# Kernel optimization log

Hardware: AMD Instinct MI355X
Metric: run time of the kernel (lower is better)

The kernel has to match this reference:

```python
import jax, jax.numpy as jnp
import numpy as np

B, S, D, H, DFF = 8, 1024, 1024, 16, 4096
DK = D // H
EPS = 1e-5


def setup_inputs() -> dict:
    key = jax.random.key(0)
    ks = jax.random.split(key, 12)
    sc = lambda n: 1.0 / np.sqrt(n)
    return {
        "x": jax.random.normal(ks[0], (B, S, D), jnp.float32),
        "src_mask": jnp.ones((B, 1, 1, S), jnp.int32),
        "wq": jax.random.normal(ks[1], (D, D), jnp.float32) * sc(D),
        "bq": jnp.zeros((D,), jnp.float32),
        "wk": jax.random.normal(ks[2], (D, D), jnp.float32) * sc(D),
        "bk": jnp.zeros((D,), jnp.float32),
        "wv": jax.random.normal(ks[3], (D, D), jnp.float32) * sc(D),
        "bv": jnp.zeros((D,), jnp.float32),
        "wo": jax.random.normal(ks[4], (D, D), jnp.float32) * sc(D),
        "bo": jnp.zeros((D,), jnp.float32),
        "w1": jax.random.normal(ks[5], (DFF, D), jnp.float32) * sc(D),
        "b1": jnp.zeros((DFF,), jnp.float32),
        "w2": jax.random.normal(ks[6], (D, DFF), jnp.float32) * sc(DFF),
        "b2": jnp.zeros((D,), jnp.float32),
        "g1": jnp.ones((1,), jnp.float32),
        "be1": jnp.zeros((1,), jnp.float32),
        "g2": jnp.ones((1,), jnp.float32),
        "be2": jnp.zeros((1,), jnp.float32),
    }


def _layernorm(x, gamma, beta):
    # Faithful to source: torch.var defaults to unbiased (ddof=1); scalar gamma/beta.
    mu = jnp.mean(x, axis=-1, keepdims=True)
    var = jnp.var(x, axis=-1, keepdims=True, ddof=1)
    return gamma * (x - mu) / jnp.sqrt(var + EPS) + beta


def _mha(x, wq, bq, wk, bk, wv, bv, wo, bo):
    q = (x @ wq.T + bq).reshape(B, S, H, DK).transpose(0, 2, 1, 3)
    k = (x @ wk.T + bk).reshape(B, S, H, DK).transpose(0, 2, 1, 3)
    v = (x @ wv.T + bv).reshape(B, S, H, DK).transpose(0, 2, 1, 3)
    scores = jnp.einsum("bhqd,bhkd->bhqk", q, k) / np.sqrt(DK)
    # NOTE: source uses non-inplace masked_fill whose result is discarded,
    # so the mask has no effect on the executed math; we replicate that.
    attn = jax.nn.softmax(scores, axis=-1)
    out = jnp.einsum("bhqk,bhkd->bhqd", attn, v)
    out = out.transpose(0, 2, 1, 3).reshape(B, S, D)
    return out @ wo.T + bo


def reference(x, src_mask, wq, bq, wk, bk, wv, bv, wo, bo,
              w1, b1, w2, b2, g1, be1, g2, be2):
    # residual 1: pre-norm self-attention (dropout=0 in eval)
    x = x + _mha(_layernorm(x, g1, be1), wq, bq, wk, bk, wv, bv, wo, bo)
    # residual 2: pre-norm FFN
    h = _layernorm(x, g2, be2)
    ff = jax.nn.relu(h @ w1.T + b1) @ w2.T + b2
    return x + ff
```

## Files before the change

### kernel.cpp

```cpp
#include <hip/hip_runtime.h>

typedef unsigned short u16;
typedef unsigned int u32;
typedef __attribute__((ext_vector_type(8))) __bf16 bf16x8;
typedef __attribute__((ext_vector_type(4))) float f32x4;

#define B_ 8
#define S_ 1024
#define D_ 1024
#define H_ 16
#define DK_ 64
#define DFF_ 4096
#define LDQKV 3072

__device__ __forceinline__ float bflo(u32 u) { return __uint_as_float(u << 16); }
__device__ __forceinline__ float bfhi(u32 u) { return __uint_as_float(u & 0xffff0000u); }
__device__ __forceinline__ u16 f2bf(float f) {
    u32 u = __float_as_uint(f);
    u += 0x7fffu + ((u >> 16) & 1u);
    return (u16)(u >> 16);
}

__device__ __forceinline__ void gl2lds16(const u16* g, u16* l) {
    __builtin_amdgcn_global_load_lds(
        (const __attribute__((address_space(1))) void*)g,
        (__attribute__((address_space(3))) void*)l, 16, 0, 0);
}

__global__ __launch_bounds__(256) void sniff_kernel(const u16* __restrict__ w,
                                                    int* __restrict__ flag) {
    float mx = 0.f;
    for (int i = threadIdx.x; i < 4096; i += 256) {
        float v = fabsf(bflo((u32)w[i]));
        if (!isnan(v)) mx = fmaxf(mx, v);
    }
#pragma unroll
    for (int m = 1; m < 64; m <<= 1) mx = fmaxf(mx, __shfl_xor(mx, m, 64));
    __shared__ float wmx[4];
    if ((threadIdx.x & 63) == 0) wmx[threadIdx.x >> 6] = mx;
    __syncthreads();
    if (threadIdx.x == 0) {
        float m2 = fmaxf(fmaxf(wmx[0], wmx[1]), fmaxf(wmx[2], wmx[3]));
        *flag = (m2 > 1e3f) ? 1 : 0;
    }
}

__global__ __launch_bounds__(256) void norm_kernel(const void* __restrict__ in,
                                                   u16* __restrict__ out, int n,
                                                   const int* __restrict__ flag) {
    const int i = blockIdx.x * 256 + threadIdx.x;
    if (i >= n) return;
    if (*flag)
        out[i] = f2bf(((const float*)in)[i]);
    else
        out[i] = ((const u16*)in)[i];
}

struct SmallTbl {
    const void* src[10];
    u16* dst[10];
    int n[10];
};
__global__ __launch_bounds__(256) void norm_small(SmallTbl tb,
                                                  const int* __restrict__ flag) {
    int i = blockIdx.x * 256 + threadIdx.x;
    const int f = *flag;
#pragma unroll
    for (int j = 0; j < 10; ++j) {
        if (i < tb.n[j]) {
            if (f)
                tb.dst[j][i] = f2bf(((const float*)tb.src[j])[i]);
            else
                tb.dst[j][i] = ((const u16*)tb.src[j])[i];
            return;
        }
        i -= tb.n[j];
    }
}

template <int INF>
__global__ __launch_bounds__(256) void ln_kernel(const void* __restrict__ in,
                                                 const u16* __restrict__ gs,
                                                 const u16* __restrict__ bs,
                                                 u16* __restrict__ out,
                                                 const int* __restrict__ flag) {
    const int row = blockIdx.x, t = threadIdx.x;
    const bool f32in = (INF == 1) || (INF == 2 && flag[0] != 0);
    float v0, v1, v2, v3;
    if (f32in) {
        const float* p = (const float*)in + (size_t)row * D_ + t * 4;
        float4 f = *(const float4*)p;
        v0 = f.x; v1 = f.y; v2 = f.z; v3 = f.w;
    } else {
        const u16* p = (const u16*)in + (size_t)row * D_ + t * 4;
        uint2 u = *(const uint2*)p;
        v0 = bflo(u.x); v1 = bfhi(u.x); v2 = bflo(u.y); v3 = bfhi(u.y);
    }
    float s = v0 + v1 + v2 + v3;
    float sq = v0 * v0 + v1 * v1 + v2 * v2 + v3 * v3;
#pragma unroll
    for (int m = 1; m < 64; m <<= 1) {
        s += __shfl_xor(s, m, 64);
        sq += __shfl_xor(sq, m, 64);
    }
    __shared__ float ss[4], sqs[4];
    const int w = t >> 6;
    if ((t & 63) == 0) { ss[w] = s; sqs[w] = sq; }
    __syncthreads();
    s = ss[0] + ss[1] + ss[2] + ss[3];
    sq = sqs[0] + sqs[1] + sqs[2] + sqs[3];
    const float mu = s * (1.f / 1024.f);
    float var = (sq - 1024.f * mu * mu) * (1.f / 1023.f);
    var = fmaxf(var, 0.f);
    const float rstd = rsqrtf(var + 1e-5f);
    const float gm = bflo((u32)gs[0]);
    const float bt = bflo((u32)bs[0]);
    const float y0 = gm * (v0 - mu) * rstd + bt;
    const float y1 = gm * (v1 - mu) * rstd + bt;
    const float y2 = gm * (v2 - mu) * rstd + bt;
    const float y3 = gm * (v3 - mu) * rstd + bt;
    uint2 uo;
    uo.x = (u32)f2bf(y0) | ((u32)f2bf(y1) << 16);
    uo.y = (u32)f2bf(y2) | ((u32)f2bf(y3) << 16);
    *(uint2*)(out + (size_t)row * D_ + t * 4) = uo;
}

template <int RELU, int RES, int OUTF>
__global__ __launch_bounds__(256, 4) void gemm_bt(const u16* __restrict__ A,
                                                  const u16* __restrict__ W,
                                                  const u16* __restrict__ bias,
                                                  const void* __restrict__ res,
                                                  void* __restrict__ out,
                                                  int M, int N, int K,
                                                  const int* __restrict__ oflag) {
    __shared__ __align__(16) u16 As[128 * 64];
    __shared__ __align__(16) u16 Bs[128 * 64];
    const int t = threadIdx.x;
    const int lane = t & 63, w = t >> 6;
    const int wm = w >> 1, wn = w & 1;

    const int nx = N >> 7;
    const int gsz = nx << 3;
    const int id = blockIdx.x;
    const int grp = id / gsz;
    const int rem = id - grp * gsz;
    const int m0 = ((grp << 3) + (rem & 7)) << 7;
    const int n0 = (rem >> 3) << 7;

    f32x4 acc[4][4];
#pragma unroll
    for (int mi = 0; mi < 4; ++mi)
#pragma unroll
        for (int ni = 0; ni < 4; ++ni) acc[mi][ni] = (f32x4){0.f, 0.f, 0.f, 0.f};

    const int r8 = lane >> 3, s8 = lane & 7;
    const int cg = s8 ^ r8;
    const u16* Ag = A + (size_t)(m0 + w * 8 + r8) * K + cg * 8;
    const u16* Bg = W + (size_t)(n0 + w * 8 + r8) * K + cg * 8;
    const size_t rI = (size_t)32 * K;
    u16* Asd = &As[(w * 8) * 64];
    u16* Bsd = &Bs[(w * 8) * 64];

    const int c = lane & 15, g = lane >> 4;
    const u16* As_r = &As[(wm * 64 + c) * 64];
    const u16* Bs_r = &Bs[(wn * 64 + c) * 64];
    const int sl0 = (g ^ (c & 7)) * 8;
    const int sl1 = ((4 + g) ^ (c & 7)) * 8;

    for (int kt = 0; kt < K; kt += 64) {
        __syncthreads();
        gl2lds16(Ag, Asd);
        gl2lds16(Ag + rI, Asd + 32 * 64);
        gl2lds16(Ag + 2 * rI, Asd + 64 * 64);
        gl2lds16(Ag + 3 * rI, Asd + 96 * 64);
        gl2lds16(Bg, Bsd);
        gl2lds16(Bg + rI, Bsd + 32 * 64);
        gl2lds16(Bg + 2 * rI, Bsd + 64 * 64);
        gl2lds16(Bg + 3 * rI, Bsd + 96 * 64);
        Ag += 64; Bg += 64;
        __syncthreads();
#pragma unroll
        for (int kc = 0; kc < 2; ++kc) {
            const int sl = kc ? sl1 : sl0;
            bf16x8 af[4], bfr[4];
#pragma unroll
            for (int i = 0; i < 4; ++i) {
                af[i] = *(const bf16x8*)(As_r + i * 16 * 64 + sl);
                bfr[i] = *(const bf16x8*)(Bs_r + i * 16 * 64 + sl);
            }
#pragma unroll
            for (int mi = 0; mi < 4; ++mi)
#pragma unroll
                for (int ni = 0; ni < 4; ++ni)
                    acc[mi][ni] = __builtin_amdgcn_mfma_f32_16x16x32_bf16(af[mi], bfr[ni], acc[mi][ni], 0, 0, 0);
        }
    }

    const int fl = oflag ? oflag[0] : 0;
    const bool f32o = (OUTF == 1) || (OUTF == 2 && fl != 0);
    const int qd = lane >> 4, cl = lane & 15;
#pragma unroll
    for (int ni = 0; ni < 4; ++ni) {
        const int col = n0 + wn * 64 + ni * 16 + cl;
        const float bv = bflo((u32)bias[col]);
#pragma unroll
        for (int mi = 0; mi < 4; ++mi) {
#pragma unroll
            for (int j = 0; j < 4; ++j) {
                const int row = m0 + wm * 64 + mi * 16 + qd * 4 + j;
                float vv = acc[mi][ni][j] + bv;
                if (RELU) vv = fmaxf(vv, 0.f);
                if (RES == 2) vv += ((const float*)res)[(size_t)row * N + col];
                if (RES == 3) {
                    if (fl)
                        vv += ((const float*)res)[(size_t)row * N + col];
                    else
                        vv += bflo((u32)((const u16*)res)[(size_t)row * N + col]);
                }
                if (f32o)
                    ((float*)out)[(size_t)row * N + col] = vv;
                else
                    ((u16*)out)[(size_t)row * N + col] = f2bf(vv);
            }
        }
    }
}

__global__ __launch_bounds__(256, 2) void attn_mfma(const u16* __restrict__ QKV,
                                                    u16* __restrict__ O) {
    __shared__ __align__(16) u16 lds[6 * 64 * 72];
    u16* Ks = lds;
    u16* VsT = lds + 64 * 72;

    const int t = threadIdx.x;
    const int lane = t & 63, w = t >> 6;
    u16* Pw = lds + (2 + w) * 64 * 72;
    const int b = blockIdx.y >> 4, h = blockIdx.y & 15;
    const int q_base = blockIdx.x * 256 + w * 64;
    const int c = lane & 15, g = lane >> 4;
    const float SC = 0.18033688011112042f;

    bf16x8 qfrag[4][2];
#pragma unroll
    for (int ni = 0; ni < 4; ++ni)
#pragma unroll
        for (int kc = 0; kc < 2; ++kc)
            qfrag[ni][kc] = *(const bf16x8*)(QKV + (size_t)(b * S_ + q_base + 16 * ni + c) * LDQKV +
                                             h * 64 + kc * 32 + 8 * g);

    f32x4 acc_o[4][4];
#pragma unroll
    for (int mi = 0; mi < 4; ++mi)
#pragma unroll
        for (int ni = 0; ni < 4; ++ni) acc_o[mi][ni] = (f32x4){0.f, 0.f, 0.f, 0.f};
    float m_st[4] = {-1e30f, -1e30f, -1e30f, -1e30f};
    float l_st[4] = {0.f, 0.f, 0.f, 0.f};

    const size_t kbase = (size_t)(b * S_) * LDQKV + 1024 + h * 64;
    const size_t vbase = (size_t)(b * S_) * LDQKV + 2048 + h * 64;
    const int srow = t >> 2, sc4 = t & 3;

    for (int kt = 0; kt < 16; ++kt) {
        __syncthreads();
        {
            const u16* kp = QKV + kbase + (size_t)(kt * 64 + srow) * LDQKV + sc4 * 16;
            uint4 k0 = *(const uint4*)kp;
            uint4 k1 = *(const uint4*)(kp + 8);
            *(uint4*)&Ks[srow * 72 + sc4 * 16] = k0;
            *(uint4*)&Ks[srow * 72 + sc4 * 16 + 8] = k1;
            const u16* vp = QKV + vbase + (size_t)(kt * 64 + srow) * LDQKV + sc4 * 16;
            uint4 v0 = *(const uint4*)vp;
            uint4 v1 = *(const uint4*)(vp + 8);
            u32 vw[8] = {v0.x, v0.y, v0.z, v0.w, v1.x, v1.y, v1.z, v1.w};
#pragma unroll
            for (int i = 0; i < 8; ++i) {
                VsT[(sc4 * 16 + 2 * i) * 72 + srow] = (u16)(vw[i] & 0xffffu);
                VsT[(sc4 * 16 + 2 * i + 1) * 72 + srow] = (u16)(vw[i] >> 16);
            }
        }
        __syncthreads();

        f32x4 acc_s[4][4];
#pragma unroll
        for (int mi = 0; mi < 4; ++mi)
#pragma unroll
            for (int ni = 0; ni < 4; ++ni) acc_s[mi][ni] = (f32x4){0.f, 0.f, 0.f, 0.f};
#pragma unroll
        for (int kc = 0; kc < 2; ++kc) {
            bf16x8 kf[4];
#pragma unroll
            for (int mi = 0; mi < 4; ++mi)
                kf[mi] = *(const bf16x8*)&Ks[(16 * mi + c) * 72 + kc * 32 + 8 * g];
#pragma unroll
            for (int mi = 0; mi < 4; ++mi)
#pragma unroll
                for (int ni = 0; ni < 4; ++ni)
                    acc_s[mi][ni] = __builtin_amdgcn_mfma_f32_16x16x32_bf16(
                        kf[mi], qfrag[ni][kc], acc_s[mi][ni], 0, 0, 0);
        }

        float alpha[4];
#pragma unroll
        for (int ni = 0; ni < 4; ++ni) {
            float mx = -1e30f;
#pragma unroll
            for (int mi = 0; mi < 4; ++mi) {
#pragma unroll
                for (int j = 0; j < 4; ++j) {
                    acc_s[mi][ni][j] *= SC;
                    mx = fmaxf(mx, acc_s[mi][ni][j]);
                }
            }
            mx = fmaxf(mx, __shfl_xor(mx, 16, 64));
            mx = fmaxf(mx, __shfl_xor(mx, 32, 64));
            const float mn = fmaxf(m_st[ni], mx);
            alpha[ni] = exp2f(m_st[ni] - mn);
            m_st[ni] = mn;
            float sum = 0.f;
#pragma unroll
            for (int mi = 0; mi < 4; ++mi) {
                float p0 = exp2f(acc_s[mi][ni][0] - mn);
                float p1 = exp2f(acc_s[mi][ni][1] - mn);
                float p2 = exp2f(acc_s[mi][ni][2] - mn);
                float p3 = exp2f(acc_s[mi][ni][3] - mn);
                sum += (p0 + p1) + (p2 + p3);
                uint2 pk;
                pk.x = (u32)f2bf(p0) | ((u32)f2bf(p1) << 16);
                pk.y = (u32)f2bf(p2) | ((u32)f2bf(p3) << 16);
                *(uint2*)&Pw[(16 * ni + c) * 72 + 16 * mi + 4 * g] = pk;
            }
            sum += __shfl_xor(sum, 16, 64);
            sum += __shfl_xor(sum, 32, 64);
            l_st[ni] = l_st[ni] * alpha[ni] + sum;
        }
#pragma unroll
        for (int mi = 0; mi < 4; ++mi)
#pragma unroll
            for (int ni = 0; ni < 4; ++ni) {
#pragma unroll
                for (int j = 0; j < 4; ++j) acc_o[mi][ni][j] *= alpha[ni];
            }

#pragma unroll
        for (int kc = 0; kc < 2; ++kc) {
            bf16x8 vf[4], pf[4];
#pragma unroll
            for (int mi = 0; mi < 4; ++mi)
                vf[mi] = *(const bf16x8*)&VsT[(16 * mi + c) * 72 + kc * 32 + 8 * g];
#pragma unroll
            for (int ni = 0; ni < 4; ++ni)
                pf[ni] = *(const bf16x8*)&Pw[(16 * ni + c) * 72 + kc * 32 + 8 * g];
#pragma unroll
            for (int mi = 0; mi < 4; ++mi)
#pragma unroll
                for (int ni = 0; ni < 4; ++ni)
                    acc_o[mi][ni] = __builtin_amdgcn_mfma_f32_16x16x32_bf16(
                        vf[mi], pf[ni], acc_o[mi][ni], 0, 0, 0);
        }
    }

#pragma unroll
    for (int ni = 0; ni < 4; ++ni) {
        const float inv_l = 1.f / l_st[ni];
        u16* op = O + (size_t)(b * S_ + q_base + 16 * ni + c) * D_ + h * 64;
#pragma unroll
        for (int mi = 0; mi < 4; ++mi) {
            uint2 uo;
            uo.x = (u32)f2bf(acc_o[mi][ni][0] * inv_l) |
                   ((u32)f2bf(acc_o[mi][ni][1] * inv_l) << 16);
            uo.y = (u32)f2bf(acc_o[mi][ni][2] * inv_l) |
                   ((u32)f2bf(acc_o[mi][ni][3] * inv_l) << 16);
            *(uint2*)(op + 16 * mi + 4 * g) = uo;
        }
    }
}

extern "C" void kernel_launch(void* const* d_in, const int* in_sizes, int n_in,
                              void* d_out, int out_size, void* d_ws, size_t ws_size,
                              hipStream_t stream) {
    (void)in_sizes; (void)n_in; (void)out_size; (void)ws_size;
    char* ws = (char*)d_ws;
    const size_t MB = 1ull << 20;
    const size_t KB = 1024;
    u16* wqkv = (u16*)(ws + 16 * MB);
    u16* won  = (u16*)(ws + 22 * MB);
    u16* w1n  = (u16*)(ws + 24 * MB);
    u16* w2n  = (u16*)(ws + 32 * MB);
    u16* bqkv = (u16*)(ws + 40 * MB);
    u16* bon  = (u16*)(ws + 40 * MB + 64 * KB);
    u16* b1n  = (u16*)(ws + 40 * MB + 128 * KB);
    u16* b2n  = (u16*)(ws + 40 * MB + 192 * KB);
    u16* g1n  = (u16*)(ws + 40 * MB + 256 * KB);
    u16* be1n = (u16*)(ws + 40 * MB + 320 * KB);
    u16* g2n  = (u16*)(ws + 40 * MB + 384 * KB);
    u16* be2n = (u16*)(ws + 40 * MB + 448 * KB);
    int* flag = (int*)(ws + 40 * MB + 512 * KB);
    u16* h1   = (u16*)(ws + 48 * MB);
    u16* qkv  = (u16*)(ws + 64 * MB);
    float* x2 = (float*)(ws + 64 * MB);
    u16* h2   = (u16*)(ws + 96 * MB);
    u16* f1   = (u16*)(ws + 112 * MB);

    const int M = B_ * S_;

    sniff_kernel<<<1, 256, 0, stream>>>((const u16*)d_in[2], flag);
    auto nrm = [&](const void* in, u16* out, int n) {
        norm_kernel<<<(n + 255) / 256, 256, 0, stream>>>(in, out, n, flag);
    };
    nrm(d_in[2],  wqkv,               D_ * D_);
    nrm(d_in[4],  wqkv + D_ * D_,     D_ * D_);
    nrm(d_in[6],  wqkv + 2 * D_ * D_, D_ * D_);
    nrm(d_in[8],  won, D_ * D_);
    nrm(d_in[10], w1n, DFF_ * D_);
    nrm(d_in[12], w2n, D_ * DFF_);
    {
        SmallTbl tb;
        tb.src[0] = d_in[3];  tb.dst[0] = bqkv;          tb.n[0] = D_;
        tb.src[1] = d_in[5];  tb.dst[1] = bqkv + D_;     tb.n[1] = D_;
        tb.src[2] = d_in[7];  tb.dst[2] = bqkv + 2 * D_; tb.n[2] = D_;
        tb.src[3] = d_in[9];  tb.dst[3] = bon;           tb.n[3] = D_;
        tb.src[4] = d_in[11]; tb.dst[4] = b1n;           tb.n[4] = DFF_;
        tb.src[5] = d_in[13]; tb.dst[5] = b2n;           tb.n[5] = D_;
        tb.src[6] = d_in[14]; tb.dst[6] = g1n;           tb.n[6] = 1;
        tb.src[7] = d_in[15]; tb.dst[7] = be1n;          tb.n[7] = 1;
        tb.src[8] = d_in[16]; tb.dst[8] = g2n;           tb.n[8] = 1;
        tb.src[9] = d_in[17]; tb.dst[9] = be2n;          tb.n[9] = 1;
        const int tot = 5 * D_ + DFF_ + 4;
        norm_small<<<(tot + 255) / 256, 256, 0, stream>>>(tb, flag);
    }

    ln_kernel<2><<<M, 256, 0, stream>>>(d_in[0], g1n, be1n, h1, flag);
    gemm_bt<0, 0, 0><<<(LDQKV / 128) * (M / 128), 256, 0, stream>>>(h1, wqkv, bqkv, nullptr, qkv, M, LDQKV, D_, flag);
    attn_mfma<<<dim3(S_ / 256, B_ * H_), 256, 0, stream>>>(qkv, h1);
    gemm_bt<0, 3, 1><<<(D_ / 128) * (M / 128), 256, 0, stream>>>(h1, won, bon, d_in[0], x2, M, D_, D_, flag);
    ln_kernel<1><<<M, 256, 0, stream>>>((const void*)x2, g2n, be2n, h2, flag);
    gemm_bt<1, 0, 0><<<(DFF_ / 128) * (M / 128), 256, 0, stream>>>(h2, w1n, b1n, nullptr, f1, M, DFF_, D_, flag);
    gemm_bt<0, 2, 2><<<(D_ / 128) * (M / 128), 256, 0, stream>>>(f1, w2n, b2n, (const void*)x2, (void*)d_out, M, D_, DFF_, flag);
}
```

Measured before the change: 553.8 us.

## Swizzle attention LDS layout, async K loads, lazy rescale, packed bf16 converts

Reworks the attention kernel's shared-memory tiles from padded 72-stride rows to XOR-swizzled 64-stride rows. K tiles now load directly into LDS with global_load_lds, and V is transposed as packed 32-bit writes. Softmax folds the scale into an fma, skips rescaling the accumulators when the row max does not change, and uses the hardware packed bf16 convert. MFMA sections also raise wave priority. The aim is fewer LDS bank conflicts and fewer VALU instructions in attention, but the swizzle index math is intricate and easy to get wrong.

```diff
diff --git a/kernel.cpp b/kernel.cpp
--- a/kernel.cpp
+++ b/kernel.cpp
@@ -19,6 +19,11 @@
     u32 u = __float_as_uint(f);
     u += 0x7fffu + ((u >> 16) & 1u);
     return (u16)(u >> 16);
+}
+__device__ __forceinline__ u32 cvtpk(float lo, float hi) {
+    u32 r;
+    asm("v_cvt_pk_bf16_f32 %0, %1, %2" : "=v"(r) : "v"(lo), "v"(hi));
+    return r;
 }
 
 __device__ __forceinline__ void gl2lds16(const u16* g, u16* l) {
@@ -228,16 +233,17 @@
 
 __global__ __launch_bounds__(256, 2) void attn_mfma(const u16* __restrict__ QKV,
                                                     u16* __restrict__ O) {
-    __shared__ __align__(16) u16 lds[6 * 64 * 72];
+    __shared__ __align__(16) u16 lds[6 * 64 * 64];
     u16* Ks = lds;
-    u16* VsT = lds + 64 * 72;
+    u16* VsT = lds + 64 * 64;
 
     const int t = threadIdx.x;
     const int lane = t & 63, w = t >> 6;
-    u16* Pw = lds + (2 + w) * 64 * 72;
+    u16* Pw = lds + (2 + w) * 64 * 64;
     const int b = blockIdx.y >> 4, h = blockIdx.y & 15;
     const int q_base = blockIdx.x * 256 + w * 64;
     const int c = lane & 15, g = lane >> 4;
+    const int c7 = c & 7;
     const float SC = 0.18033688011112042f;
 
     bf16x8 qfrag[4][2];
@@ -258,24 +264,40 @@
 
     const size_t kbase = (size_t)(b * S_) * LDQKV + 1024 + h * 64;
     const size_t vbase = (size_t)(b * S_) * LDQKV + 2048 + h * 64;
-    const int srow = t >> 2, sc4 = t & 3;
+
+    const int r8 = lane >> 3, s8 = lane & 7;
+    const int cgk = s8 ^ r8;
+    const u16* Kg = QKV + kbase + (size_t)(w * 8 + r8) * LDQKV + cgk * 8;
+    u16* Ksd = &Ks[(w * 8) * 64];
+    const size_t rIk = (size_t)32 * LDQKV;
+
+    const int vr = t >> 3, vdq = t & 7;
+    const u16* Vg = QKV + vbase + (size_t)(2 * vr) * LDQKV + vdq * 8;
+
+    int vfx[4];
+#pragma unroll
+    for (int mi = 0; mi < 4; ++mi) vfx[mi] = c7 ^ ((2 * mi + (c >> 3)) & 7);
 
     for (int kt = 0; kt < 16; ++kt) {
         __syncthreads();
+        gl2lds16(Kg, Ksd);
+        gl2lds16(Kg + rIk, Ksd + 32 * 64);
+        Kg += (size_t)64 * LDQKV;
         {
-            const u16* kp = QKV + kbase + (size_t)(kt * 64 + srow) * LDQKV + sc4 * 16;
-            uint4 k0 = *(const uint4*)kp;
-            uint4 k1 = *(const uint4*)(kp + 8);
-            *(uint4*)&Ks[srow * 72 + sc4 * 16] = k0;
-            *(uint4*)&Ks[srow * 72 + sc4 * 16 + 8] = k1;
-            const u16* vp = QKV + vbase + (size_t)(kt * 64 + srow) * LDQKV + sc4 * 16;
-            uint4 v0 = *(const uint4*)vp;
-            uint4 v1 = *(const uint4*)(vp + 8);
-            u32 vw[8] = {v0.x, v0.y, v0.z, v0.w, v1.x, v1.y, v1.z, v1.w};
+            uint4 a = *(const uint4*)Vg;
+            uint4 bb = *(const uint4*)(Vg + LDQKV);
+            Vg += (size_t)64 * LDQKV;
+            const u32 aw[4] = {a.x, a.y, a.z, a.w};
+            const u32 bw[4] = {bb.x, bb.y, bb.z, bb.w};
 #pragma unroll
             for (int i = 0; i < 8; ++i) {
-                VsT[(sc4 * 16 + 2 * i) * 72 + srow] = (u16)(vw[i] & 0xffffu);
-                VsT[(sc4 * 16 + 2 * i + 1) * 72 + srow] = (u16)(vw[i] >> 16);
+                u32 wv;
+                if (i & 1)
+                    wv = (aw[i >> 1] >> 16) | (bw[i >> 1] & 0xffff0000u);
+                else
+                    wv = (aw[i >> 1] & 0xffffu) | (bw[i >> 1] << 16);
+                const int d = vdq * 8 + i;
+                *(u32*)&VsT[d * 64 + (((vr >> 2) ^ (i ^ vdq)) << 3) + ((vr & 3) << 1)] = wv;
             }
         }
         __syncthreads();
@@ -285,12 +307,13 @@
         for (int mi = 0; mi < 4; ++mi)
 #pragma unroll
             for (int ni = 0; ni < 4; ++ni) acc_s[mi][ni] = (f32x4){0.f, 0.f, 0.f, 0.f};
+        __builtin_amdgcn_s_setprio(1);
 #pragma unroll
         for (int kc = 0; kc < 2; ++kc) {
             bf16x8 kf[4];
 #pragma unroll
             for (int mi = 0; mi < 4; ++mi)
-                kf[mi] = *(const bf16x8*)&Ks[(16 * mi + c) * 72 + kc * 32 + 8 * g];
+                kf[mi] = *(const bf16x8*)&Ks[(16 * mi + c) * 64 + (((kc * 4 + g) ^ c7) << 3)];
 #pragma unroll
             for (int mi = 0; mi < 4; ++mi)
 #pragma unroll
@@ -298,58 +321,69 @@
                     acc_s[mi][ni] = __builtin_amdgcn_mfma_f32_16x16x32_bf16(
                         kf[mi], qfrag[ni][kc], acc_s[mi][ni], 0, 0, 0);
         }
+        __builtin_amdgcn_s_setprio(0);
 
         float alpha[4];
+        bool resc[4];
 #pragma unroll
         for (int ni = 0; ni < 4; ++ni) {
             float mx = -1e30f;
 #pragma unroll
             for (int mi = 0; mi < 4; ++mi) {
 #pragma unroll
-                for (int j = 0; j < 4; ++j) {
-                    acc_s[mi][ni][j] *= SC;
-                    mx = fmaxf(mx, acc_s[mi][ni][j]);
-                }
+                for (int j = 0; j < 4; ++j) mx = fmaxf(mx, acc_s[mi][ni][j]);
             }
             mx = fmaxf(mx, __shfl_xor(mx, 16, 64));
             mx = fmaxf(mx, __shfl_xor(mx, 32, 64));
-            const float mn = fmaxf(m_st[ni], mx);
-            alpha[ni] = exp2f(m_st[ni] - mn);
-            m_st[ni] = mn;
+            const float mo = m_st[ni];
+            const float mn = fmaxf(mo, mx);
+            resc[ni] = __any(mn > mo);
+            if (resc[ni]) {
+                alpha[ni] = exp2f((mo - mn) * SC);
+                m_st[ni] = mn;
+            } else {
+                alpha[ni] = 1.f;
+            }
+            const float nms = m_st[ni] * SC;
             float sum = 0.f;
 #pragma unroll
             for (int mi = 0; mi < 4; ++mi) {
-                float p0 = exp2f(acc_s[mi][ni][0] - mn);
-                float p1 = exp2f(acc_s[mi][ni][1] - mn);
-                float p2 = exp2f(acc_s[mi][ni][2] - mn);
-                float p3 = exp2f(acc_s[mi][ni][3] - mn);
+                const float p0 = exp2f(fmaf(acc_s[mi][ni][0], SC, -nms));
+                const float p1 = exp2f(fmaf(acc_s[mi][ni][1], SC, -nms));
+                const float p2 = exp2f(fmaf(acc_s[mi][ni][2], SC, -nms));
+                const float p3 = exp2f(fmaf(acc_s[mi][ni][3], SC, -nms));
                 sum += (p0 + p1) + (p2 + p3);
                 uint2 pk;
-                pk.x = (u32)f2bf(p0) | ((u32)f2bf(p1) << 16);
-                pk.y = (u32)f2bf(p2) | ((u32)f2bf(p3) << 16);
-                *(uint2*)&Pw[(16 * ni + c) * 72 + 16 * mi + 4 * g] = pk;
+                pk.x = cvtpk(p0, p1);
+                pk.y = cvtpk(p2, p3);
+                *(uint2*)&Pw[(16 * ni + c) * 64 +
+                             ((((2 * mi + (g >> 1)) ^ c7) << 3) + ((g & 1) << 2))] = pk;
             }
             sum += __shfl_xor(sum, 16, 64);
             sum += __shfl_xor(sum, 32, 64);
-            l_st[ni] = l_st[ni] * alpha[ni] + sum;
-        }
-#pragma unroll
-        for (int mi = 0; mi < 4; ++mi)
-#pragma unroll
-            for (int ni = 0; ni < 4; ++ni) {
-#pragma unroll
-                for (int j = 0; j < 4; ++j) acc_o[mi][ni][j] *= alpha[ni];
-            }
-
+            l_st[ni] = (resc[ni] ? l_st[ni] * alpha[ni] : l_st[ni]) + sum;
+        }
+#pragma unroll
+        for (int ni = 0; ni < 4; ++ni) {
+            if (resc[ni]) {
+#pragma unroll
+                for (int mi = 0; mi < 4; ++mi) {
+#pragma unroll
+                    for (int j = 0; j < 4; ++j) acc_o[mi][ni][j] *= alpha[ni];
+                }
+            }
+        }
+
+        __builtin_amdgcn_s_setprio(1);
 #pragma unroll
         for (int kc = 0; kc < 2; ++kc) {
             bf16x8 vf[4], pf[4];
 #pragma unroll
             for (int mi = 0; mi < 4; ++mi)
-                vf[mi] = *(const bf16x8*)&VsT[(16 * mi + c) * 72 + kc * 32 + 8 * g];
+                vf[mi] = *(const bf16x8*)&VsT[(16 * mi + c) * 64 + (((kc * 4 + g) ^ vfx[mi]) << 3)];
 #pragma unroll
             for (int ni = 0; ni < 4; ++ni)
-                pf[ni] = *(const bf16x8*)&Pw[(16 * ni + c) * 72 + kc * 32 + 8 * g];
+                pf[ni] = *(const bf16x8*)&Pw[(16 * ni + c) * 64 + (((kc * 4 + g) ^ c7) << 3)];
 #pragma unroll
             for (int mi = 0; mi < 4; ++mi)
 #pragma unroll
@@ -357,6 +391,7 @@
                     acc_o[mi][ni] = __builtin_amdgcn_mfma_f32_16x16x32_bf16(
                         vf[mi], pf[ni], acc_o[mi][ni], 0, 0, 0);
         }
+        __builtin_amdgcn_s_setprio(0);
     }
 
 #pragma unroll
@@ -366,10 +401,8 @@
 #pragma unroll
         for (int mi = 0; mi < 4; ++mi) {
             uint2 uo;
-            uo.x = (u32)f2bf(acc_o[mi][ni][0] * inv_l) |
-                   ((u32)f2bf(acc_o[mi][ni][1] * inv_l) << 16);
-            uo.y = (u32)f2bf(acc_o[mi][ni][2] * inv_l) |
-                   ((u32)f2bf(acc_o[mi][ni][3] * inv_l) << 16);
+            uo.x = cvtpk(acc_o[mi][ni][0] * inv_l, acc_o[mi][ni][1] * inv_l);
+            uo.y = cvtpk(acc_o[mi][ni][2] * inv_l, acc_o[mi][ni][3] * inv_l);
             *(uint2*)(op + 16 * mi + 4 * g) = uo;
         }
     }
```

New measurement: 539.7 us. 2.5% less time.
